# Optimization experiments

Measured on AMD Instinct MI355X. Metric: run time of the kernel, lower is better.

Reference implementation:

```python
import jax, jax.numpy as jnp
import numpy as np

N = 30000
E = 300000
DIN, DH, DOUT, L = 256, 128, 64, 6


def setup_inputs() -> dict:
    key = jax.random.key(0)
    ks = jax.random.split(key, 8)
    feats = jax.random.normal(ks[0], (N, DIN), dtype=jnp.float32)
    src = jax.random.randint(ks[1], (E,), 0, N, dtype=jnp.int32)
    dst = jax.random.randint(ks[2], (E,), 0, N, dtype=jnp.int32)
    W0 = jax.random.normal(ks[3], (DIN, DH), dtype=jnp.float32) * 0.05
    b0 = jnp.zeros((DH,), dtype=jnp.float32)
    Wh = jax.random.normal(ks[4], (L, DH, DH), dtype=jnp.float32) * 0.05
    bh = jnp.zeros((L, DH), dtype=jnp.float32)
    Wout = jax.random.normal(ks[5], (DH * (L + 1), DOUT), dtype=jnp.float32) * 0.05
    bout = jnp.zeros((DOUT,), dtype=jnp.float32)
    return {"feats": feats, "src": src, "dst": dst, "W0": W0, "b0": b0,
            "Wh": Wh, "bh": bh, "Wout": Wout, "bout": bout}


def _graph_conv(x, W, b, src, dst, inv_sqrt_out, inv_sqrt_in):
    # DGL GraphConv, norm='both': D_out^{-1/2} -> sum over edges -> D_in^{-1/2} -> XW+b -> relu
    x = x * inv_sqrt_out[:, None]
    m = jax.ops.segment_sum(x[src], dst, num_segments=N)  # [N, d]
    m = m * inv_sqrt_in[:, None]
    return jax.nn.relu(m @ W + b)


def reference(feats, src, dst, W0, b0, Wh, bh, Wout, bout):
    ones = jnp.ones((E,), dtype=jnp.float32)
    out_deg = jax.ops.segment_sum(ones, src, num_segments=N)
    in_deg = jax.ops.segment_sum(ones, dst, num_segments=N)
    inv_sqrt_out = jax.lax.rsqrt(jnp.clip(out_deg, 1.0))
    inv_sqrt_in = jax.lax.rsqrt(jnp.clip(in_deg, 1.0))

    h = _graph_conv(feats, W0, b0, src, dst, inv_sqrt_out, inv_sqrt_in)
    reps = [h]
    for i in range(L):
        h = _graph_conv(h, Wh[i], bh[i], src, dst, inv_sqrt_out, inv_sqrt_in)
        reps.append(h)
    jk = jnp.concatenate(reps, axis=-1)  # [N, DH*(L+1)]
    # update_all(copy_u, sum): un-normalized neighborhood sum
    h = jax.ops.segment_sum(jk[src], dst, num_segments=N)
    return h @ Wout + bout
```

## Files before the change

kernel.cpp:

```cpp
#include <hip/hip_runtime.h>

#define NN 30000
#define NE 300000
#define D_IN 256
#define D_H 128
#define D_OUT 64
#define NL 6
#define NB ((NN + 255) / 256)

typedef unsigned short ushort_t;
typedef unsigned int uint_t;
typedef __attribute__((ext_vector_type(8))) short sh8;
typedef __attribute__((ext_vector_type(4))) float f4;

static __device__ __forceinline__ ushort_t f2bf(float f) {
    uint_t u = __float_as_uint(f);
    u = (u + 0x7FFFu + ((u >> 16) & 1u)) >> 16;
    return (ushort_t)u;
}

__global__ void degree_kernel(const int* __restrict__ src, const int* __restrict__ dst,
                              int* __restrict__ outdeg, int* __restrict__ indeg) {
    int e = blockIdx.x * blockDim.x + threadIdx.x;
    if (e < NE) {
        atomicAdd(&outdeg[src[e]], 1);
        atomicAdd(&indeg[dst[e]], 1);
    }
}

__global__ void rsqrt_kernel(const int* __restrict__ deg, float* __restrict__ inv, int n) {
    int i = blockIdx.x * blockDim.x + threadIdx.x;
    if (i < n) {
        float d = (float)deg[i];
        inv[i] = rsqrtf(d < 1.0f ? 1.0f : d);
    }
}

__global__ __launch_bounds__(256) void bsum_kernel(const int* __restrict__ deg,
                                                   int* __restrict__ bsum) {
    __shared__ int wsum[4];
    int t = threadIdx.x, lane = t & 63, w = t >> 6;
    int i = blockIdx.x * 256 + t;
    int v = (i < NN) ? deg[i] : 0;
#pragma unroll
    for (int off = 32; off; off >>= 1) v += __shfl_down(v, off, 64);
    if (lane == 0) wsum[w] = v;
    __syncthreads();
    if (t == 0) bsum[blockIdx.x] = wsum[0] + wsum[1] + wsum[2] + wsum[3];
}

__global__ __launch_bounds__(128) void boffs_kernel(const int* __restrict__ bsum,
                                                    int* __restrict__ boffs,
                                                    int* __restrict__ row_ptr) {
    __shared__ int wtot[2];
    int t = threadIdx.x, lane = t & 63, w = t >> 6;
    int v = (t < NB) ? bsum[t] : 0;
    int s = v;
#pragma unroll
    for (int off = 1; off < 64; off <<= 1) {
        int x = __shfl_up(s, off, 64);
        if (lane >= off) s += x;
    }
    if (lane == 63) wtot[w] = s;
    __syncthreads();
    int add = (w == 1) ? wtot[0] : 0;
    if (t < NB) boffs[t] = add + s - v;
    if (t == 0) row_ptr[NN] = NE;
}

__global__ __launch_bounds__(256) void rowptr_kernel(const int* __restrict__ deg,
                                                     const int* __restrict__ boffs,
                                                     int* __restrict__ row_ptr) {
    __shared__ int wsum[4];
    int t = threadIdx.x, lane = t & 63, w = t >> 6;
    int i = blockIdx.x * 256 + t;
    int v = (i < NN) ? deg[i] : 0;
    int s = v;
#pragma unroll
    for (int off = 1; off < 64; off <<= 1) {
        int x = __shfl_up(s, off, 64);
        if (lane >= off) s += x;
    }
    if (lane == 63) wsum[w] = s;
    __syncthreads();
    int woff = 0;
#pragma unroll
    for (int k = 0; k < 4; k++)
        if (k < w) woff += wsum[k];
    if (i < NN) row_ptr[i] = boffs[blockIdx.x] + woff + s - v;
}

__global__ void fill_kernel(const int* __restrict__ src, const int* __restrict__ dst,
                            const int* __restrict__ row_ptr, int* __restrict__ cursor,
                            int* __restrict__ col) {
    int e = blockIdx.x * blockDim.x + threadIdx.x;
    if (e < NE) {
        int d = dst[e];
        int pos = atomicAdd(&cursor[d], 1);
        col[row_ptr[d] + pos] = src[e];
    }
}

__global__ void packw_kernel(const float* __restrict__ W0,
                             const float* __restrict__ Wh,
                             const float* __restrict__ Wout,
                             ushort_t* __restrict__ W0p,
                             ushort_t* __restrict__ Whp,
                             ushort_t* __restrict__ Woutp) {
    int g = blockIdx.x * blockDim.x + threadIdx.x;
    int frag = g >> 6;
    int lane = g & 63;
    if (frag >= 368) return;
    const float* srcw;
    ushort_t* dstp;
    int fl, KF, M;
    if (frag < 64) {
        fl = frag; KF = 8; M = 128;
        srcw = W0;
        dstp = W0p;
    } else if (frag < 64 + 192) {
        int f2 = frag - 64;
        int l = f2 / 32; fl = f2 % 32; KF = 4; M = 128;
        srcw = Wh + (size_t)l * D_H * D_H;
        dstp = Whp + (size_t)l * 32 * 512;
    } else {
        int f2 = frag - 256;
        int l = f2 / 16; fl = f2 % 16; KF = 4; M = 64;
        srcw = Wout + (size_t)l * D_H * D_OUT;
        dstp = Woutp + (size_t)l * 16 * 512;
    }
    int ct = fl / KF;
    int kt = fl % KF;
    int krow = kt * 32 + (lane >> 4) * 8;
    int cidx = ct * 16 + (lane & 15);
    ushort_t tmp[8];
#pragma unroll
    for (int j = 0; j < 8; j++)
        tmp[j] = f2bf(srcw[(size_t)(krow + j) * M + cidx]);
    uint4 o;
    o.x = (uint_t)tmp[0] | ((uint_t)tmp[1] << 16);
    o.y = (uint_t)tmp[2] | ((uint_t)tmp[3] << 16);
    o.z = (uint_t)tmp[4] | ((uint_t)tmp[5] << 16);
    o.w = (uint_t)tmp[6] | ((uint_t)tmp[7] << 16);
    *(uint4*)(dstp + (size_t)fl * 512 + lane * 8) = o;
}

__global__ __launch_bounds__(256) void gemm0_kernel(
    const float* __restrict__ X,
    const ushort_t* __restrict__ W1p,
    const float* __restrict__ scale,
    ushort_t* __restrict__ Tb)
{
    constexpr int KF = 8;
    const int lane = threadIdx.x & 63;
    const int w = threadIdx.x >> 6;
    const int rg = w >> 1;
    const int cgrp = w & 1;
    const int row0 = blockIdx.x * 32 + rg * 16;

    int arow = row0 + (lane & 15);
    if (arow >= NN) arow = NN - 1;
    const float* xr = X + (size_t)arow * D_IN + ((lane >> 4) * 8);
    sh8 a[KF];
#pragma unroll
    for (int kt = 0; kt < KF; kt++) {
        float4 lo = *(const float4*)(xr + kt * 32);
        float4 hi = *(const float4*)(xr + kt * 32 + 4);
        sh8 t;
        t[0] = (short)f2bf(lo.x); t[1] = (short)f2bf(lo.y);
        t[2] = (short)f2bf(lo.z); t[3] = (short)f2bf(lo.w);
        t[4] = (short)f2bf(hi.x); t[5] = (short)f2bf(hi.y);
        t[6] = (short)f2bf(hi.z); t[7] = (short)f2bf(hi.w);
        a[kt] = t;
    }

    const int crow0 = row0 + (lane >> 4) * 4;
    float s[4];
#pragma unroll
    for (int r = 0; r < 4; r++) {
        int rw = crow0 + r;
        s[r] = scale[rw < NN ? rw : NN - 1];
    }
#pragma unroll
    for (int i = 0; i < 4; i++) {
        int ct = cgrp * 4 + i;
        f4 acc = {0.f, 0.f, 0.f, 0.f};
        const ushort_t* wp = W1p + ((size_t)(ct * KF) << 9) + lane * 8;
#pragma unroll
        for (int kt = 0; kt < KF; kt++)
            acc = __builtin_amdgcn_mfma_f32_16x16x32_bf16(
                a[kt], *(const sh8*)(wp + ((size_t)kt << 9)), acc, 0, 0, 0);
        int colb = ct * 16 + (lane & 15);
#pragma unroll
        for (int r = 0; r < 4; r++) {
            int rw = crow0 + r;
            if (rw < NN)
                Tb[(size_t)rw * 128 + colb] = f2bf(acc[r] * s[r]);
        }
    }
}

static __device__ __forceinline__ void acc8(float* acc, uint4 u) {
    uint_t wv[4] = {u.x, u.y, u.z, u.w};
#pragma unroll
    for (int i = 0; i < 4; i++) {
        acc[2 * i]     += __uint_as_float(wv[i] << 16);
        acc[2 * i + 1] += __uint_as_float(wv[i] & 0xFFFF0000u);
    }
}

template <bool HAS_T, bool HAS_P>
__global__ __launch_bounds__(64, 4) void fused_kernel(
    const ushort_t* __restrict__ Tin,
    const int* __restrict__ row_ptr,
    const int* __restrict__ col,
    const float* __restrict__ inv_in,
    const float* __restrict__ bias,
    const ushort_t* __restrict__ W1p,
    const ushort_t* __restrict__ W2p,
    const float* __restrict__ inv_out,
    ushort_t* __restrict__ Tout,
    float* __restrict__ P)
{
    const int lane = threadIdx.x & 63;
    const int row0 = blockIdx.x * 16;
    int r = row0 + (lane & 15);
    int rc = r < NN ? r : NN - 1;
    const int beg = row_ptr[rc];
    const int end = row_ptr[rc + 1];
    const int cb = (lane >> 4) * 8;
    const int cq = (lane >> 4) * 4;

    float acc[4][8];
#pragma unroll
    for (int kt = 0; kt < 4; kt++)
#pragma unroll
        for (int i = 0; i < 8; i++) acc[kt][i] = 0.f;

    const uint_t* T32 = (const uint_t*)Tin;
    int j = beg;
    for (; j + 1 < end; j += 2) {
        int c0 = col[j], c1 = col[j + 1];
        const uint_t* p0 = T32 + (size_t)c0 * 64 + cq;
        const uint_t* p1 = T32 + (size_t)c1 * 64 + cq;
        uint4 u00 = *(const uint4*)(p0);
        uint4 u01 = *(const uint4*)(p0 + 16);
        uint4 u02 = *(const uint4*)(p0 + 32);
        uint4 u03 = *(const uint4*)(p0 + 48);
        uint4 u10 = *(const uint4*)(p1);
        uint4 u11 = *(const uint4*)(p1 + 16);
        uint4 u12 = *(const uint4*)(p1 + 32);
        uint4 u13 = *(const uint4*)(p1 + 48);
        acc8(acc[0], u00); acc8(acc[0], u10);
        acc8(acc[1], u01); acc8(acc[1], u11);
        acc8(acc[2], u02); acc8(acc[2], u12);
        acc8(acc[3], u03); acc8(acc[3], u13);
    }
    if (j < end) {
        int c0 = col[j];
        const uint_t* p0 = T32 + (size_t)c0 * 64 + cq;
        acc8(acc[0], *(const uint4*)(p0));
        acc8(acc[1], *(const uint4*)(p0 + 16));
        acc8(acc[2], *(const uint4*)(p0 + 32));
        acc8(acc[3], *(const uint4*)(p0 + 48));
    }

    const float s = inv_in[rc];
    sh8 a[4];
#pragma unroll
    for (int kt = 0; kt < 4; kt++) {
        float4 b0 = *(const float4*)(bias + kt * 32 + cb);
        float4 b1 = *(const float4*)(bias + kt * 32 + cb + 4);
        float bb[8] = {b0.x, b0.y, b0.z, b0.w, b1.x, b1.y, b1.z, b1.w};
        sh8 t;
#pragma unroll
        for (int i = 0; i < 8; i++) {
            float h = fmaxf(fmaf(acc[kt][i], s, bb[i]), 0.f);
            t[i] = (short)f2bf(h);
        }
        a[kt] = t;
    }

    const int crow0 = row0 + (lane >> 4) * 4;

    if (HAS_T) {
        float sc[4];
#pragma unroll
        for (int rr = 0; rr < 4; rr++) {
            int cr = crow0 + rr;
            sc[rr] = inv_out[cr < NN ? cr : NN - 1];
        }
#pragma unroll
        for (int ct = 0; ct < 8; ct++) {
            f4 accT = {0.f, 0.f, 0.f, 0.f};
            const ushort_t* wp = W1p + ((size_t)(ct * 4) << 9) + lane * 8;
#pragma unroll
            for (int kt = 0; kt < 4; kt++)
                accT = __builtin_amdgcn_mfma_f32_16x16x32_bf16(
                    a[kt], *(const sh8*)(wp + ((size_t)kt << 9)), accT, 0, 0, 0);
            int colb = ct * 16 + (lane & 15);
#pragma unroll
            for (int rr = 0; rr < 4; rr++) {
                int cr = crow0 + rr;
                if (cr < NN)
                    Tout[(size_t)cr * 128 + colb] = f2bf(accT[rr] * sc[rr]);
            }
        }
    }
    if (HAS_P) {
#pragma unroll
        for (int ct = 0; ct < 4; ct++) {
            f4 accP = {0.f, 0.f, 0.f, 0.f};
            const ushort_t* wp = W2p + ((size_t)(ct * 4) << 9) + lane * 8;
#pragma unroll
            for (int kt = 0; kt < 4; kt++)
                accP = __builtin_amdgcn_mfma_f32_16x16x32_bf16(
                    a[kt], *(const sh8*)(wp + ((size_t)kt << 9)), accP, 0, 0, 0);
            int colb = ct * 16 + (lane & 15);
#pragma unroll
            for (int rr = 0; rr < 4; rr++) {
                int cr = crow0 + rr;
                if (cr < NN)
                    P[(size_t)cr * 64 + colb] += accP[rr];
            }
        }
    }
}

__global__ __launch_bounds__(256) void gather_f32_kernel(
    const float* __restrict__ P,
    const int* __restrict__ row_ptr,
    const int* __restrict__ col,
    const float* __restrict__ bias,
    float* __restrict__ Y) {
    int idx = blockIdx.x * blockDim.x + threadIdx.x;
    int node = idx >> 4;
    int q = idx & 15;
    if (node >= NN) return;
    int beg = row_ptr[node];
    int end = row_ptr[node + 1];
    float4 acc = make_float4(0.f, 0.f, 0.f, 0.f);
    int j = beg;
    for (; j + 3 < end; j += 4) {
        int c0 = col[j], c1 = col[j + 1], c2 = col[j + 2], c3 = col[j + 3];
        float4 v0 = *(const float4*)(P + (size_t)c0 * 64 + q * 4);
        float4 v1 = *(const float4*)(P + (size_t)c1 * 64 + q * 4);
        float4 v2 = *(const float4*)(P + (size_t)c2 * 64 + q * 4);
        float4 v3 = *(const float4*)(P + (size_t)c3 * 64 + q * 4);
        acc.x += (v0.x + v1.x) + (v2.x + v3.x);
        acc.y += (v0.y + v1.y) + (v2.y + v3.y);
        acc.z += (v0.z + v1.z) + (v2.z + v3.z);
        acc.w += (v0.w + v1.w) + (v2.w + v3.w);
    }
    for (; j < end; j++) {
        int c0 = col[j];
        float4 v0 = *(const float4*)(P + (size_t)c0 * 64 + q * 4);
        acc.x += v0.x; acc.y += v0.y; acc.z += v0.z; acc.w += v0.w;
    }
    float4 b = *(const float4*)(bias + q * 4);
    acc.x += b.x; acc.y += b.y; acc.z += b.z; acc.w += b.w;
    *(float4*)(Y + (size_t)node * 64 + q * 4) = acc;
}

extern "C" void kernel_launch(void* const* d_in, const int* in_sizes, int n_in,
                              void* d_out, int out_size, void* d_ws, size_t ws_size,
                              hipStream_t stream) {
    const float* feats = (const float*)d_in[0];
    const int*   src   = (const int*)d_in[1];
    const int*   dst   = (const int*)d_in[2];
    const float* W0    = (const float*)d_in[3];
    const float* b0    = (const float*)d_in[4];
    const float* Wh    = (const float*)d_in[5];
    const float* bh    = (const float*)d_in[6];
    const float* Wout  = (const float*)d_in[7];
    const float* bout  = (const float*)d_in[8];
    float* out = (float*)d_out;

    float* ws      = (float*)d_ws;
    float* inv_out = ws;
    float* inv_in  = ws + NN;
    float* p       = ws + 2 * NN;
    ushort_t* tb   = (ushort_t*)(p + (size_t)NN * 64);
    ushort_t* ha   = tb + (size_t)NN * 128;
    ushort_t* hb   = ha + (size_t)NN * 128;
    ushort_t* fb   = hb + (size_t)NN * 128;
    ushort_t* w0p  = fb + (size_t)NN * 256;
    ushort_t* whp  = w0p + 64 * 512;
    ushort_t* wop  = whp + 192 * 512;
    int* ibase     = (int*)(wop + 112 * 512);
    int* outdeg_i  = ibase;
    int* indeg_i   = ibase + NN;
    int* row_ptr   = ibase + 2 * NN;
    int* cursor    = ibase + 3 * NN + 1;
    int* col       = ibase + 4 * NN + 1;
    int* bsum      = (int*)hb;
    int* boffs     = bsum + NB + 8;

    const int B = 256;
    const int fused_blocks = (NN + 15) / 16;
    const int gather_blocks = (NN * 16 + B - 1) / B;

    hipMemsetAsync(outdeg_i, 0, 2 * NN * sizeof(int), stream);
    hipMemsetAsync(cursor, 0, NN * sizeof(int), stream);
    hipMemsetAsync(p, 0, (size_t)NN * D_OUT * sizeof(float), stream);
    degree_kernel<<<(NE + B - 1) / B, B, 0, stream>>>(src, dst, outdeg_i, indeg_i);
    rsqrt_kernel<<<(2 * NN + B - 1) / B, B, 0, stream>>>(outdeg_i, inv_out, 2 * NN);
    bsum_kernel<<<NB, 256, 0, stream>>>(indeg_i, bsum);
    boffs_kernel<<<1, 128, 0, stream>>>(bsum, boffs, row_ptr);
    rowptr_kernel<<<NB, 256, 0, stream>>>(indeg_i, boffs, row_ptr);
    fill_kernel<<<(NE + B - 1) / B, B, 0, stream>>>(src, dst, row_ptr, cursor, col);
    packw_kernel<<<(368 * 64 + B - 1) / B, B, 0, stream>>>(W0, Wh, Wout, w0p, whp, wop);

    gemm0_kernel<<<(NN + 31) / 32, 256, 0, stream>>>(feats, w0p, inv_out, tb);

    const ushort_t* tcur = tb;
    ushort_t* tnext = ha;
    for (int l = 0; l < NL; l++) {
        const float* bias_l = (l == 0) ? b0 : bh + (size_t)(l - 1) * D_H;
        fused_kernel<true, true><<<fused_blocks, 64, 0, stream>>>(
            tcur, row_ptr, col, inv_in, bias_l,
            whp + (size_t)l * 32 * 512, wop + (size_t)l * 16 * 512,
            inv_out, tnext, p);
        const ushort_t* t = tcur; tcur = tnext; tnext = (ushort_t*)t;
    }
    fused_kernel<false, true><<<fused_blocks, 64, 0, stream>>>(
        tcur, row_ptr, col, inv_in, bh + (size_t)(NL - 1) * D_H,
        nullptr, wop + (size_t)NL * 16 * 512, nullptr, nullptr, p);

    gather_f32_kernel<<<gather_blocks, B, 0, stream>>>(p, row_ptr, col, bout, out);
}
```

Measured before the change: 369.0 us.

## Split fused layer edge gather across four waves with LDS reduction

The fused gather+GEMM kernel now runs 256 threads per 16-row block. Each of four wavefronts gathers a quarter of each row's neighbor list, and the partial sums are reduced through a 32KB shared buffer. The 12 MFMA output tiles (8 for the next layer's T, 4 for the P projection) are then spread across the waves instead of one wave doing all of them. This buys more memory-level parallelism per row and shorter per-wave serial work, at the cost of LDS traffic, a barrier and redundant accumulation. The bounds checks on rows were dropped, which relies on NN being a multiple of 16.

```diff
diff --git a/kernel.cpp b/kernel.cpp
--- a/kernel.cpp
+++ b/kernel.cpp
@@ -210,7 +210,7 @@
 }
 
 template <bool HAS_T, bool HAS_P>
-__global__ __launch_bounds__(64, 4) void fused_kernel(
+__global__ __launch_bounds__(256, 4) void fused4_kernel(
     const ushort_t* __restrict__ Tin,
     const int* __restrict__ row_ptr,
     const int* __restrict__ col,
@@ -222,15 +222,21 @@
     ushort_t* __restrict__ Tout,
     float* __restrict__ P)
 {
-    const int lane = threadIdx.x & 63;
+    __shared__ float part[4 * 32 * 64];
+    const int tid = threadIdx.x;
+    const int lane = tid & 63;
+    const int w = tid >> 6;
     const int row0 = blockIdx.x * 16;
-    int r = row0 + (lane & 15);
-    int rc = r < NN ? r : NN - 1;
-    const int beg = row_ptr[rc];
-    const int end = row_ptr[rc + 1];
+    const int r = row0 + (lane & 15);
+    const int beg = row_ptr[r];
+    const int end = row_ptr[r + 1];
     const int cb = (lane >> 4) * 8;
     const int cq = (lane >> 4) * 4;
 
+    const int cnt = end - beg;
+    const int j0 = beg + ((cnt * w) >> 2);
+    const int j1 = beg + ((cnt * (w + 1)) >> 2);
+
     float acc[4][8];
 #pragma unroll
     for (int kt = 0; kt < 4; kt++)
@@ -238,8 +244,8 @@
         for (int i = 0; i < 8; i++) acc[kt][i] = 0.f;
 
     const uint_t* T32 = (const uint_t*)Tin;
-    int j = beg;
-    for (; j + 1 < end; j += 2) {
+    int j = j0;
+    for (; j + 1 < j1; j += 2) {
         int c0 = col[j], c1 = col[j + 1];
         const uint_t* p0 = T32 + (size_t)c0 * 64 + cq;
         const uint_t* p1 = T32 + (size_t)c1 * 64 + cq;
@@ -256,7 +262,7 @@
         acc8(acc[2], u02); acc8(acc[2], u12);
         acc8(acc[3], u03); acc8(acc[3], u13);
     }
-    if (j < end) {
+    if (j < j1) {
         int c0 = col[j];
         const uint_t* p0 = T32 + (size_t)c0 * 64 + cq;
         acc8(acc[0], *(const uint4*)(p0));
@@ -265,7 +271,24 @@
         acc8(acc[3], *(const uint4*)(p0 + 48));
     }
 
-    const float s = inv_in[rc];
+#pragma unroll
+    for (int kt = 0; kt < 4; kt++)
+#pragma unroll
+        for (int i = 0; i < 8; i++)
+            part[(w * 32 + kt * 8 + i) * 64 + lane] = acc[kt][i];
+    __syncthreads();
+
+#pragma unroll
+    for (int ow = 1; ow < 4; ow++) {
+        int w2 = (w + ow) & 3;
+#pragma unroll
+        for (int kt = 0; kt < 4; kt++)
+#pragma unroll
+            for (int i = 0; i < 8; i++)
+                acc[kt][i] += part[(w2 * 32 + kt * 8 + i) * 64 + lane];
+    }
+
+    const float s = inv_in[r];
     sh8 a[4];
 #pragma unroll
     for (int kt = 0; kt < 4; kt++) {
@@ -286,44 +309,49 @@
     if (HAS_T) {
         float sc[4];
 #pragma unroll
-        for (int rr = 0; rr < 4; rr++) {
-            int cr = crow0 + rr;
-            sc[rr] = inv_out[cr < NN ? cr : NN - 1];
-        }
-#pragma unroll
-        for (int ct = 0; ct < 8; ct++) {
-            f4 accT = {0.f, 0.f, 0.f, 0.f};
-            const ushort_t* wp = W1p + ((size_t)(ct * 4) << 9) + lane * 8;
-#pragma unroll
-            for (int kt = 0; kt < 4; kt++)
-                accT = __builtin_amdgcn_mfma_f32_16x16x32_bf16(
-                    a[kt], *(const sh8*)(wp + ((size_t)kt << 9)), accT, 0, 0, 0);
-            int colb = ct * 16 + (lane & 15);
-#pragma unroll
-            for (int rr = 0; rr < 4; rr++) {
-                int cr = crow0 + rr;
-                if (cr < NN)
-                    Tout[(size_t)cr * 128 + colb] = f2bf(accT[rr] * sc[rr]);
+        for (int rr = 0; rr < 4; rr++)
+            sc[rr] = inv_out[crow0 + rr];
+#pragma unroll
+        for (int u = 0; u < 3; u++) {
+            int unit = w * 3 + u;
+            if (unit < 8) {
+                int ct = unit;
+                f4 accT = {0.f, 0.f, 0.f, 0.f};
+                const ushort_t* wp = W1p + ((size_t)(ct * 4) << 9) + lane * 8;
+#pragma unroll
+                for (int kt = 0; kt < 4; kt++)
+                    accT = __builtin_amdgcn_mfma_f32_16x16x32_bf16(
+                        a[kt], *(const sh8*)(wp + ((size_t)kt << 9)), accT, 0, 0, 0);
+                int colb = ct * 16 + (lane & 15);
+#pragma unroll
+                for (int rr = 0; rr < 4; rr++)
+                    Tout[(size_t)(crow0 + rr) * 128 + colb] = f2bf(accT[rr] * sc[rr]);
+            } else {
+                int ct = unit - 8;
+                f4 accP = {0.f, 0.f, 0.f, 0.f};
+                const ushort_t* wp = W2p + ((size_t)(ct * 4) << 9) + lane * 8;
+#pragma unroll
+                for (int kt = 0; kt < 4; kt++)
+                    accP = __builtin_amdgcn_mfma_f32_16x16x32_bf16(
+                        a[kt], *(const sh8*)(wp + ((size_t)kt << 9)), accP, 0, 0, 0);
+                int colb = ct * 16 + (lane & 15);
+#pragma unroll
+                for (int rr = 0; rr < 4; rr++)
+                    P[(size_t)(crow0 + rr) * 64 + colb] += accP[rr];
             }
         }
-    }
-    if (HAS_P) {
-#pragma unroll
-        for (int ct = 0; ct < 4; ct++) {
-            f4 accP = {0.f, 0.f, 0.f, 0.f};
-            const ushort_t* wp = W2p + ((size_t)(ct * 4) << 9) + lane * 8;
-#pragma unroll
-            for (int kt = 0; kt < 4; kt++)
-                accP = __builtin_amdgcn_mfma_f32_16x16x32_bf16(
-                    a[kt], *(const sh8*)(wp + ((size_t)kt << 9)), accP, 0, 0, 0);
-            int colb = ct * 16 + (lane & 15);
-#pragma unroll
-            for (int rr = 0; rr < 4; rr++) {
-                int cr = crow0 + rr;
-                if (cr < NN)
-                    P[(size_t)cr * 64 + colb] += accP[rr];
-            }
-        }
+    } else if (HAS_P) {
+        int ct = w;
+        f4 accP = {0.f, 0.f, 0.f, 0.f};
+        const ushort_t* wp = W2p + ((size_t)(ct * 4) << 9) + lane * 8;
+#pragma unroll
+        for (int kt = 0; kt < 4; kt++)
+            accP = __builtin_amdgcn_mfma_f32_16x16x32_bf16(
+                a[kt], *(const sh8*)(wp + ((size_t)kt << 9)), accP, 0, 0, 0);
+        int colb = ct * 16 + (lane & 15);
+#pragma unroll
+        for (int rr = 0; rr < 4; rr++)
+            P[(size_t)(crow0 + rr) * 64 + colb] += accP[rr];
     }
 }
 
@@ -417,13 +445,13 @@
     ushort_t* tnext = ha;
     for (int l = 0; l < NL; l++) {
         const float* bias_l = (l == 0) ? b0 : bh + (size_t)(l - 1) * D_H;
-        fused_kernel<true, true><<<fused_blocks, 64, 0, stream>>>(
+        fused4_kernel<true, true><<<fused_blocks, 256, 0, stream>>>(
             tcur, row_ptr, col, inv_in, bias_l,
             whp + (size_t)l * 32 * 512, wop + (size_t)l * 16 * 512,
             inv_out, tnext, p);
         const ushort_t* t = tcur; tcur = tnext; tnext = (ushort_t*)t;
     }
-    fused_kernel<false, true><<<fused_blocks, 64, 0, stream>>>(
+    fused4_kernel<false, true><<<fused_blocks, 256, 0, stream>>>(
         tcur, row_ptr, col, inv_in, bh + (size_t)(NL - 1) * D_H,
         nullptr, wop + (size_t)NL * 16 * 512, nullptr, nullptr, p);
 
```

Result: faster. 332.7 us (-9.8%).
